# Kernel tuning notes

Hardware: AMD Instinct MI355X
Metric: run time of the kernel (lower is better)

Reference implementation:

```python
import jax, jax.numpy as jnp
import numpy as np
import math

N = 100000   # nodes
E = 1600000  # edges (avg degree 16)
D = 128      # in_dim == out_dim
H = 8        # heads
DK = D // H  # 16


def setup_inputs() -> dict:
    key = jax.random.key(0)
    ks = jax.random.split(key, 16)
    s = 1.0 / math.sqrt(D)
    inp = {
        "h": jax.random.normal(ks[0], (N, D), dtype=jnp.float32),
        "src": jax.random.randint(ks[1], (E,), 0, N, dtype=jnp.int32),
        "dst": jax.random.randint(ks[2], (E,), 0, N, dtype=jnp.int32),
        # linear params (torch Linear: y = x @ W.T + b)
        "Wk": jax.random.normal(ks[3], (D, D), dtype=jnp.float32) * s,
        "bk": jnp.zeros((D,), dtype=jnp.float32),
        "Wq": jax.random.normal(ks[4], (D, D), dtype=jnp.float32) * s,
        "bq": jnp.zeros((D,), dtype=jnp.float32),
        "Wv": jax.random.normal(ks[5], (D, D), dtype=jnp.float32) * s,
        "bv": jnp.zeros((D,), dtype=jnp.float32),
        "Wa": jax.random.normal(ks[6], (D, D), dtype=jnp.float32) * s,
        "ba": jnp.zeros((D,), dtype=jnp.float32),
        # relation params
        "rel_att": jax.random.normal(ks[7], (H, DK, DK), dtype=jnp.float32) * (1.0 / math.sqrt(DK)),
        "rel_msg": jax.random.normal(ks[8], (H, DK, DK), dtype=jnp.float32) * (1.0 / math.sqrt(DK)),
        "rel_pri": jnp.ones((H,), dtype=jnp.float32),
        "skip": jnp.ones((1,), dtype=jnp.float32),
    }
    return inp


def reference(h, src, dst, Wk, bk, Wq, bq, Wv, bv, Wa, ba, rel_att, rel_msg, rel_pri, skip):
    sqrt_dk = math.sqrt(DK)
    # per-node projections -> [N, H, DK]
    k = (h @ Wk.T + bk).reshape(N, H, DK)
    q = (h @ Wq.T + bq).reshape(N, H, DK)
    v = (h @ Wv.T + bv).reshape(N, H, DK)
    # per-relation transforms on k and v
    k = jnp.einsum('nhd,hde->nhe', k, rel_att)
    v = jnp.einsum('nhd,hde->nhe', v, rel_msg)
    # edge scores: dot(q[dst], k[src]) per head -> [E, H]
    score = jnp.einsum('ehd,ehd->eh', q[dst], k[src])
    score = score * rel_pri / sqrt_dk
    # edge softmax normalized over incoming edges of each dst node
    smax = jax.ops.segment_max(score, dst, num_segments=N)        # [N, H]
    ex = jnp.exp(score - smax[dst])                               # [E, H]
    denom = jax.ops.segment_sum(ex, dst, num_segments=N)         # [N, H]
    attn = ex / denom[dst]                                       # [E, H]
    # weighted scatter-aggregation of source values
    msg = v[src] * attn[:, :, None]                               # [E, H, DK]
    t = jax.ops.segment_sum(msg, dst, num_segments=N)             # [N, H, DK]
    t = t.reshape(N, D)
    # target-specific aggregation with learned skip gate (dropout=0 eval, norm=Identity)
    trans_out = t @ Wa.T + ba
    alpha = jax.nn.sigmoid(skip[0])
    new_h = trans_out * alpha + h * (1.0 - alpha)
    return new_h
```

## Files before the change

### kernel.cpp

```cpp
#include <hip/hip_runtime.h>
#include <hip/hip_bf16.h>
#include <math.h>

#define NN 100000
#define EE 1600000
#define DD 128
#define HH 8
#define LDW 136
#define BSH 9
#define NB 196
#define EPB 8192

typedef short short8 __attribute__((ext_vector_type(8)));
typedef float f32x4 __attribute__((ext_vector_type(4)));

__device__ __forceinline__ unsigned short f2bf(float f) {
    unsigned int u = __float_as_uint(f);
    u += 0x7fffu + ((u >> 16) & 1u);
    return (unsigned short)(u >> 16);
}
__device__ __forceinline__ float bf2f(unsigned short h) {
    return __uint_as_float((unsigned int)h << 16);
}
__device__ __forceinline__ void cvt8(const float4& a, const float4& b,
                                     short8& h8, short8& l8) {
    float vals[8] = {a.x, a.y, a.z, a.w, b.x, b.y, b.z, b.w};
    #pragma unroll
    for (int j = 0; j < 8; j++) {
        unsigned short hi = f2bf(vals[j]);
        h8[j] = (short)hi;
        l8[j] = (short)f2bf(vals[j] - bf2f(hi));
    }
}

__global__ void prep_weights(const float* __restrict__ Wq, const float* __restrict__ Wk,
                             const float* __restrict__ Wv, const float* __restrict__ Wa,
                             const float* __restrict__ bq, const float* __restrict__ bk,
                             const float* __restrict__ bv, const float* __restrict__ ba,
                             const float* __restrict__ rel_att, const float* __restrict__ rel_msg,
                             unsigned short* __restrict__ WH, unsigned short* __restrict__ WL,
                             float* __restrict__ BE) {
    int o = blockIdx.x * 256 + threadIdx.x;
    int j = o >> 7, c = o & 127;
    int which = blockIdx.y;
    float val;
    if (which == 0) {
        val = Wq[o];
        if (o < 128) BE[o] = bq[o];
    } else if (which == 3) {
        val = Wa[o];
        if (o < 128) BE[384 + o] = ba[o];
    } else {
        const float* rel = (which == 1) ? rel_att : rel_msg;
        const float* W   = (which == 1) ? Wk : Wv;
        const float* b   = (which == 1) ? bk : bv;
        int hh = j >> 4, e = j & 15;
        val = 0.f;
        #pragma unroll
        for (int d = 0; d < 16; d++)
            val += rel[hh * 256 + d * 16 + e] * W[(hh * 16 + d) * 128 + c];
        if (c == 0) {
            float bacc = 0.f;
            #pragma unroll
            for (int d = 0; d < 16; d++)
                bacc += b[hh * 16 + d] * rel[hh * 256 + d * 16 + e];
            BE[which * 128 + j] = bacc;
        }
    }
    unsigned short hi = f2bf(val);
    unsigned short lo = f2bf(val - bf2f(hi));
    WH[which * 16384 + o] = hi;
    WL[which * 16384 + o] = lo;
}

__launch_bounds__(256, 2)
__global__ void gemm_reg(const float* __restrict__ x,
                         const unsigned short* __restrict__ WH,
                         const unsigned short* __restrict__ WL,
                         const float* __restrict__ BE, int nw,
                         float* __restrict__ out0, unsigned short* __restrict__ kvout,
                         const float* __restrict__ resid, const float* __restrict__ skip) {
    __shared__ unsigned short wh[128 * LDW];
    __shared__ unsigned short wl[128 * LDW];
    int tid = threadIdx.x;
    int wv = tid >> 6, lane = tid & 63;
    int lrow = lane & 15, quad = lane >> 4;
    int base = blockIdx.x * 128;

    short8 ah[2][4], al[2][4];
    float4 fz = {0.f, 0.f, 0.f, 0.f};
    #pragma unroll
    for (int mt = 0; mt < 2; mt++) {
        int row = base + wv * 32 + mt * 16 + lrow;
        const float* xr = x + (size_t)row * 128;
        bool ok = (row < NN);
        #pragma unroll
        for (int kc = 0; kc < 4; kc++) {
            int off = kc * 32 + quad * 8;
            float4 a = ok ? *(const float4*)&xr[off] : fz;
            float4 b = ok ? *(const float4*)&xr[off + 4] : fz;
            cvt8(a, b, ah[mt][kc], al[mt][kc]);
        }
    }

    float alpha = 1.f, beta = 0.f;
    if (resid) {
        float sv = skip[0];
        alpha = 1.f / (1.f + expf(-sv));
        beta = 1.f - alpha;
    }

    for (int wi = 0; wi < nw; wi++) {
        __syncthreads();
        const unsigned short* WHp = WH + wi * 16384;
        const unsigned short* WLp = WL + wi * 16384;
        for (int i = tid; i < 128 * 16; i += 256) {
            int n = i >> 4, kq = (i & 15) << 3;
            *(uint4*)&wh[n * LDW + kq] = *(const uint4*)&WHp[n * 128 + kq];
            *(uint4*)&wl[n * LDW + kq] = *(const uint4*)&WLp[n * 128 + kq];
        }
        __syncthreads();

        f32x4 zero4 = {0.f, 0.f, 0.f, 0.f};
        f32x4 acc[2][8];
        #pragma unroll
        for (int a = 0; a < 2; a++)
            #pragma unroll
            for (int b = 0; b < 8; b++) acc[a][b] = zero4;

        #pragma unroll
        for (int kc = 0; kc < 4; kc++) {
            #pragma unroll
            for (int nt = 0; nt < 8; nt++) {
                int koff = kc * 32 + quad * 8;
                int brow = (nt * 16 + lrow) * LDW + koff;
                short8 bh = *(const short8*)&wh[brow];
                short8 bl = *(const short8*)&wl[brow];
                acc[0][nt] = __builtin_amdgcn_mfma_f32_16x16x32_bf16(ah[0][kc], bh, acc[0][nt], 0, 0, 0);
                acc[1][nt] = __builtin_amdgcn_mfma_f32_16x16x32_bf16(ah[1][kc], bh, acc[1][nt], 0, 0, 0);
                acc[0][nt] = __builtin_amdgcn_mfma_f32_16x16x32_bf16(al[0][kc], bh, acc[0][nt], 0, 0, 0);
                acc[1][nt] = __builtin_amdgcn_mfma_f32_16x16x32_bf16(al[1][kc], bh, acc[1][nt], 0, 0, 0);
                acc[0][nt] = __builtin_amdgcn_mfma_f32_16x16x32_bf16(ah[0][kc], bl, acc[0][nt], 0, 0, 0);
                acc[1][nt] = __builtin_amdgcn_mfma_f32_16x16x32_bf16(ah[1][kc], bl, acc[1][nt], 0, 0, 0);
            }
        }

        const float* be = BE + wi * 128;
        #pragma unroll
        for (int nt = 0; nt < 8; nt++) {
            int col = nt * 16 + lrow;
            float bb = be[col];
            #pragma unroll
            for (int mt = 0; mt < 2; mt++) {
                int r0 = base + wv * 32 + mt * 16 + quad * 4;
                #pragma unroll
                for (int rg = 0; rg < 4; rg++) {
                    int row = r0 + rg;
                    if (row < NN) {
                        float val = acc[mt][nt][rg] + bb;
                        if (wi == 0) {
                            if (resid) val = alpha * val + beta * resid[(size_t)row * 128 + col];
                            out0[(size_t)row * 128 + col] = val;
                        } else {
                            int pos = ((col >> 2) << 3) + ((wi - 1) << 2) + (col & 3);
                            kvout[(size_t)row * 256 + pos] = f2bf(val);
                        }
                    }
                }
            }
        }
    }
}

__global__ void bucket_hist(const int* __restrict__ dst, int* __restrict__ bcnt) {
    __shared__ int lh[NB];
    int t = threadIdx.x;
    for (int i = t; i < NB; i += 256) lh[i] = 0;
    __syncthreads();
    int base = blockIdx.x * EPB;
    int cnt = min(EPB, EE - base);
    for (int i = t; i < cnt; i += 256)
        atomicAdd(&lh[dst[base + i] >> BSH], 1);
    __syncthreads();
    for (int i = t; i < NB; i += 256)
        if (lh[i]) atomicAdd(&bcnt[i], lh[i]);
}

__global__ void bucket_scan(const int* __restrict__ bcnt, int* __restrict__ btail,
                            int* __restrict__ sbase) {
    __shared__ int buf[2][256];
    int t = threadIdx.x;
    int v = (t < NB) ? bcnt[t] : 0;
    buf[0][t] = v;
    __syncthreads();
    int sb = 0;
    #pragma unroll
    for (int d = 1; d < 256; d <<= 1) {
        int x = buf[sb][t];
        if (t >= d) x += buf[sb][t - d];
        buf[sb ^ 1][t] = x;
        __syncthreads();
        sb ^= 1;
    }
    if (t < NB) {
        int excl = buf[sb][t] - v;
        btail[t] = excl;
        sbase[t] = excl;
    }
    if (t == 0) sbase[NB] = EE;
}

__launch_bounds__(256, 1)
__global__ void bucket_scatter(const int* __restrict__ src, const int* __restrict__ dst,
                               int* __restrict__ btail, int* __restrict__ packed) {
    __shared__ int2 staged[EPB];
    __shared__ int hist[NB], lstart[NB], cursor[NB], gbase[NB];
    __shared__ int sbuf[2][256];
    int t = threadIdx.x;
    for (int i = t; i < NB; i += 256) hist[i] = 0;
    __syncthreads();
    int base = blockIdx.x * EPB;
    int cnt = min(EPB, EE - base);
    for (int i = t; i < cnt; i += 256)
        atomicAdd(&hist[dst[base + i] >> BSH], 1);
    __syncthreads();
    int v = (t < NB) ? hist[t] : 0;
    sbuf[0][t] = v;
    __syncthreads();
    int sb = 0;
    #pragma unroll
    for (int d = 1; d < 256; d <<= 1) {
        int x = sbuf[sb][t];
        if (t >= d) x += sbuf[sb][t - d];
        sbuf[sb ^ 1][t] = x;
        __syncthreads();
        sb ^= 1;
    }
    if (t < NB) {
        lstart[t] = sbuf[sb][t] - v;
        cursor[t] = sbuf[sb][t] - v;
    }
    __syncthreads();
    for (int i = t; i < cnt; i += 256) {
        int d = dst[base + i], s = src[base + i];
        int r = atomicAdd(&cursor[d >> BSH], 1);
        staged[r] = make_int2(s, d);
    }
    __syncthreads();
    for (int i = t; i < NB; i += 256) {
        int c = hist[i];
        if (c) gbase[i] = atomicAdd(&btail[i], c);
    }
    __syncthreads();
    for (int i = t; i < cnt; i += 256) {
        int2 e = staged[i];
        int b = e.y >> BSH;
        packed[gbase[b] + (i - lstart[b])] = ((e.y & 511) << 17) | e.x;
    }
}

__launch_bounds__(512, 2)
__global__ void node_sort(const int* __restrict__ packed, const int* __restrict__ sbase,
                          int* __restrict__ offs, int* __restrict__ sorted_src) {
    __shared__ int hist[512], cursor[512];
    __shared__ int scn[2][512];
    int t = threadIdx.x;
    int b = blockIdx.x;
    int s0 = sbase[b], s1 = sbase[b + 1];
    hist[t] = 0;
    __syncthreads();
    for (int e = s0 + t; e < s1; e += 512)
        atomicAdd(&hist[packed[e] >> 17], 1);
    __syncthreads();
    int v = hist[t];
    scn[0][t] = v;
    __syncthreads();
    int sb = 0;
    #pragma unroll
    for (int d = 1; d < 512; d <<= 1) {
        int x = scn[sb][t];
        if (t >= d) x += scn[sb][t - d];
        scn[sb ^ 1][t] = x;
        __syncthreads();
        sb ^= 1;
    }
    int incl = scn[sb][t];
    int node = (b << BSH) + t;
    if (node < NN) offs[node] = s0 + incl;
    cursor[t] = s0 + incl - v;
    __syncthreads();
    for (int e = s0 + t; e < s1; e += 512) {
        int p = packed[e];
        int pos = atomicAdd(&cursor[p >> 17], 1);
        sorted_src[pos] = p & 0x1FFFF;
    }
}

__launch_bounds__(256, 8)
__global__ void fused_attn(const float* __restrict__ q,
                           const unsigned short* __restrict__ kv,
                           const int* __restrict__ offs, const int* __restrict__ sorted_src,
                           const float* __restrict__ rel_pri, float* __restrict__ t) {
    int wave = threadIdx.x >> 6, lane = threadIdx.x & 63;
    int n = blockIdx.x * 4 + wave;
    if (n >= NN) return;
    int half = lane >> 5;
    int sl = lane & 31;
    int hh = sl >> 2;
    int start = (n > 0) ? offs[n - 1] : 0;
    int cnt = offs[n] - start;

    float4 q4 = *(const float4*)&q[(size_t)n * 128 + sl * 4];
    float scale = rel_pri[hh] * 0.25f * 1.44269504088896340736f;
    q4.x *= scale; q4.y *= scale; q4.z *= scale; q4.w *= scale;

    const unsigned short* kvp = kv + sl * 8;

    float4 o4 = {0.f, 0.f, 0.f, 0.f};
    float denom = 0.f;

    int nIter = (cnt + 1) >> 1;
    #pragma unroll 4
    for (int it = 0; it < nIter; it++) {
        int j = 2 * it + half;
        float wgt = (j < cnt) ? 1.f : 0.f;
        int jj = (j < cnt) ? j : (cnt - 1);
        int s = sorted_src[start + jj];
        uint4 kvb = *(const uint4*)(kvp + (size_t)s * 256);
        float p = q4.x * bf2f((unsigned short)(kvb.x & 0xffff))
                + q4.y * bf2f((unsigned short)(kvb.x >> 16))
                + q4.z * bf2f((unsigned short)(kvb.y & 0xffff))
                + q4.w * bf2f((unsigned short)(kvb.y >> 16));
        p += __shfl_xor(p, 1);
        p += __shfl_xor(p, 2);
        float e = __builtin_amdgcn_exp2f(p) * wgt;
        denom += e;
        o4.x = fmaf(bf2f((unsigned short)(kvb.z & 0xffff)), e, o4.x);
        o4.y = fmaf(bf2f((unsigned short)(kvb.z >> 16)),    e, o4.y);
        o4.z = fmaf(bf2f((unsigned short)(kvb.w & 0xffff)), e, o4.z);
        o4.w = fmaf(bf2f((unsigned short)(kvb.w >> 16)),    e, o4.w);
    }

    denom += __shfl_xor(denom, 32);
    o4.x += __shfl_xor(o4.x, 32);
    o4.y += __shfl_xor(o4.y, 32);
    o4.z += __shfl_xor(o4.z, 32);
    o4.w += __shfl_xor(o4.w, 32);

    if (half == 0) {
        float inv = (cnt > 0) ? 1.f / denom : 0.f;
        o4.x *= inv; o4.y *= inv; o4.z *= inv; o4.w *= inv;
        *(float4*)&t[(size_t)n * 128 + sl * 4] = o4;
    }
}

extern "C" void kernel_launch(void* const* d_in, const int* in_sizes, int n_in,
                              void* d_out, int out_size, void* d_ws, size_t ws_size,
                              hipStream_t stream) {
    const float* h    = (const float*)d_in[0];
    const int*   src  = (const int*)d_in[1];
    const int*   dst  = (const int*)d_in[2];
    const float* Wk   = (const float*)d_in[3];
    const float* bk   = (const float*)d_in[4];
    const float* Wq   = (const float*)d_in[5];
    const float* bq   = (const float*)d_in[6];
    const float* Wv   = (const float*)d_in[7];
    const float* bv   = (const float*)d_in[8];
    const float* Wa   = (const float*)d_in[9];
    const float* ba   = (const float*)d_in[10];
    const float* rel_att = (const float*)d_in[11];
    const float* rel_msg = (const float*)d_in[12];
    const float* rel_pri = (const float*)d_in[13];
    const float* skip    = (const float*)d_in[14];
    float* out = (float*)d_out;

    unsigned short* kvbuf = (unsigned short*)d_ws;
    float* BE   = (float*)(kvbuf + (size_t)NN * 256);
    int* scratch = (int*)(BE + 512);
    int* bcnt  = scratch;
    int* btail = bcnt + NB;
    int* sbase = btail + NB;
    int* offs  = scratch + NN;
    int* bsum  = offs + NN;
    int* sorted_src = bsum + 128;
    unsigned short* WH = (unsigned short*)(sorted_src + EE);
    unsigned short* WL = WH + 4 * 16384;
    int* packed = (int*)kvbuf;
    float* q = out;
    float* t = out;

    const int A_BLOCKS = (EE + EPB - 1) / EPB;
    const int GEMM_BLOCKS = (NN + 127) / 128;

    prep_weights<<<dim3(64, 4), 256, 0, stream>>>(Wq, Wk, Wv, Wa, bq, bk, bv, ba,
                                                  rel_att, rel_msg, WH, WL, BE);
    hipMemsetAsync(bcnt, 0, NB * sizeof(int), stream);
    bucket_hist<<<A_BLOCKS, 256, 0, stream>>>(dst, bcnt);
    bucket_scan<<<1, 256, 0, stream>>>(bcnt, btail, sbase);
    bucket_scatter<<<A_BLOCKS, 256, 0, stream>>>(src, dst, btail, packed);
    node_sort<<<NB, 512, 0, stream>>>(packed, sbase, offs, sorted_src);

    gemm_reg<<<GEMM_BLOCKS, 256, 0, stream>>>(h, WH, WL, BE, 3, q, kvbuf,
                                              nullptr, nullptr);
    fused_attn<<<(NN + 3) / 4, 256, 0, stream>>>(q, kvbuf, offs, sorted_src,
                                                 rel_pri, t);
    gemm_reg<<<GEMM_BLOCKS, 256, 0, stream>>>(t, WH + 3 * 16384, WL + 3 * 16384,
                                              BE + 384, 1, out, nullptr,
                                              h, skip);
}
```

Before: 494.8 us.

## Merge weight prep with histogram and bucket scatter with QKV GEMM launches

Weight preparation and the dst histogram now run as one launch, using block-index ranges to pick the work. When the workspace is large enough, the packed edge buffer gets its own region, so the bucket scatter and the QKV projection GEMM can share one launch and run concurrently. The attention kernel now has each wave process four nodes in sequence, which cuts the block count. These changes reduce launch overhead and idle tails, but the merged kernel's shared-memory footprint and occupancy are set by the larger of the two roles, and the dependent path only runs if the workspace is big enough.

Result: no change. 493.3 us (-0.3%).

```diff
diff --git a/kernel.cpp b/kernel.cpp
--- a/kernel.cpp
+++ b/kernel.cpp
@@ -10,6 +10,8 @@
 #define BSH 9
 #define NB 196
 #define EPB 8192
+#define A_BLOCKS 196
+#define GEMM_BLOCKS 782
 
 typedef short short8 __attribute__((ext_vector_type(8)));
 typedef float f32x4 __attribute__((ext_vector_type(4)));
@@ -33,16 +35,16 @@
     }
 }
 
-__global__ void prep_weights(const float* __restrict__ Wq, const float* __restrict__ Wk,
+__device__ __forceinline__ void prep_work(int which, int bx,
+                             const float* __restrict__ Wq, const float* __restrict__ Wk,
                              const float* __restrict__ Wv, const float* __restrict__ Wa,
                              const float* __restrict__ bq, const float* __restrict__ bk,
                              const float* __restrict__ bv, const float* __restrict__ ba,
                              const float* __restrict__ rel_att, const float* __restrict__ rel_msg,
                              unsigned short* __restrict__ WH, unsigned short* __restrict__ WL,
                              float* __restrict__ BE) {
-    int o = blockIdx.x * 256 + threadIdx.x;
+    int o = bx * 256 + threadIdx.x;
     int j = o >> 7, c = o & 127;
-    int which = blockIdx.y;
     float val;
     if (which == 0) {
         val = Wq[o];
@@ -73,19 +75,45 @@
     WL[which * 16384 + o] = lo;
 }
 
-__launch_bounds__(256, 2)
-__global__ void gemm_reg(const float* __restrict__ x,
+__global__ void prep_hist(const float* __restrict__ Wq, const float* __restrict__ Wk,
+                          const float* __restrict__ Wv, const float* __restrict__ Wa,
+                          const float* __restrict__ bq, const float* __restrict__ bk,
+                          const float* __restrict__ bv, const float* __restrict__ ba,
+                          const float* __restrict__ rel_att, const float* __restrict__ rel_msg,
+                          unsigned short* __restrict__ WH, unsigned short* __restrict__ WL,
+                          float* __restrict__ BE,
+                          const int* __restrict__ dst, int* __restrict__ bcnt) {
+    __shared__ int lh[NB];
+    int bid = blockIdx.x;
+    if (bid < 256) {
+        prep_work(bid >> 6, bid & 63, Wq, Wk, Wv, Wa, bq, bk, bv, ba,
+                  rel_att, rel_msg, WH, WL, BE);
+    } else {
+        int t = threadIdx.x;
+        for (int i = t; i < NB; i += 256) lh[i] = 0;
+        __syncthreads();
+        int base = (bid - 256) * EPB;
+        int cnt = min(EPB, EE - base);
+        for (int i = t; i < cnt; i += 256)
+            atomicAdd(&lh[dst[base + i] >> BSH], 1);
+        __syncthreads();
+        for (int i = t; i < NB; i += 256)
+            if (lh[i]) atomicAdd(&bcnt[i], lh[i]);
+    }
+}
+
+__device__ __forceinline__ void gemm_body(char* smemc, int base,
+                         const float* __restrict__ x,
                          const unsigned short* __restrict__ WH,
                          const unsigned short* __restrict__ WL,
                          const float* __restrict__ BE, int nw,
                          float* __restrict__ out0, unsigned short* __restrict__ kvout,
                          const float* __restrict__ resid, const float* __restrict__ skip) {
-    __shared__ unsigned short wh[128 * LDW];
-    __shared__ unsigned short wl[128 * LDW];
+    unsigned short* wh = (unsigned short*)smemc;
+    unsigned short* wl = wh + 128 * LDW;
     int tid = threadIdx.x;
     int wv = tid >> 6, lane = tid & 63;
     int lrow = lane & 15, quad = lane >> 4;
-    int base = blockIdx.x * 128;
 
     short8 ah[2][4], al[2][4];
     float4 fz = {0.f, 0.f, 0.f, 0.f};
@@ -172,18 +200,15 @@
     }
 }
 
-__global__ void bucket_hist(const int* __restrict__ dst, int* __restrict__ bcnt) {
-    __shared__ int lh[NB];
-    int t = threadIdx.x;
-    for (int i = t; i < NB; i += 256) lh[i] = 0;
-    __syncthreads();
-    int base = blockIdx.x * EPB;
-    int cnt = min(EPB, EE - base);
-    for (int i = t; i < cnt; i += 256)
-        atomicAdd(&lh[dst[base + i] >> BSH], 1);
-    __syncthreads();
-    for (int i = t; i < NB; i += 256)
-        if (lh[i]) atomicAdd(&bcnt[i], lh[i]);
+__launch_bounds__(256, 2)
+__global__ void gemm_reg(const float* __restrict__ x,
+                         const unsigned short* __restrict__ WH,
+                         const unsigned short* __restrict__ WL,
+                         const float* __restrict__ BE, int nw,
+                         float* __restrict__ out0, unsigned short* __restrict__ kvout,
+                         const float* __restrict__ resid, const float* __restrict__ skip) {
+    __shared__ __align__(16) char smem[69632];
+    gemm_body(smem, blockIdx.x * 128, x, WH, WL, BE, nw, out0, kvout, resid, skip);
 }
 
 __global__ void bucket_scan(const int* __restrict__ bcnt, int* __restrict__ btail,
@@ -210,35 +235,38 @@
     if (t == 0) sbase[NB] = EE;
 }
 
-__launch_bounds__(256, 1)
-__global__ void bucket_scatter(const int* __restrict__ src, const int* __restrict__ dst,
+__device__ __forceinline__ void scatter_work(char* smemc, int bid,
+                               const int* __restrict__ src, const int* __restrict__ dst,
                                int* __restrict__ btail, int* __restrict__ packed) {
-    __shared__ int2 staged[EPB];
-    __shared__ int hist[NB], lstart[NB], cursor[NB], gbase[NB];
-    __shared__ int sbuf[2][256];
+    int2* staged = (int2*)smemc;
+    int* hist   = (int*)(smemc + 65536);
+    int* lstart = hist + NB;
+    int* cursor = lstart + NB;
+    int* gbase  = cursor + NB;
+    int* sbuf   = gbase + NB;
     int t = threadIdx.x;
     for (int i = t; i < NB; i += 256) hist[i] = 0;
     __syncthreads();
-    int base = blockIdx.x * EPB;
+    int base = bid * EPB;
     int cnt = min(EPB, EE - base);
     for (int i = t; i < cnt; i += 256)
         atomicAdd(&hist[dst[base + i] >> BSH], 1);
     __syncthreads();
     int v = (t < NB) ? hist[t] : 0;
-    sbuf[0][t] = v;
+    sbuf[t] = v;
     __syncthreads();
     int sb = 0;
     #pragma unroll
     for (int d = 1; d < 256; d <<= 1) {
-        int x = sbuf[sb][t];
-        if (t >= d) x += sbuf[sb][t - d];
-        sbuf[sb ^ 1][t] = x;
+        int x = sbuf[sb * 256 + t];
+        if (t >= d) x += sbuf[sb * 256 + t - d];
+        sbuf[(sb ^ 1) * 256 + t] = x;
         __syncthreads();
         sb ^= 1;
     }
     if (t < NB) {
-        lstart[t] = sbuf[sb][t] - v;
-        cursor[t] = sbuf[sb][t] - v;
+        lstart[t] = sbuf[sb * 256 + t] - v;
+        cursor[t] = sbuf[sb * 256 + t] - v;
     }
     __syncthreads();
     for (int i = t; i < cnt; i += 256) {
@@ -257,6 +285,29 @@
         int b = e.y >> BSH;
         packed[gbase[b] + (i - lstart[b])] = ((e.y & 511) << 17) | e.x;
     }
+}
+
+__launch_bounds__(256, 1)
+__global__ void bucket_scatter(const int* __restrict__ src, const int* __restrict__ dst,
+                               int* __restrict__ btail, int* __restrict__ packed) {
+    __shared__ __align__(16) char smem[70720];
+    scatter_work(smem, blockIdx.x, src, dst, btail, packed);
+}
+
+__launch_bounds__(256, 2)
+__global__ void gemm0_scatter(const float* __restrict__ x,
+                              const unsigned short* __restrict__ WH,
+                              const unsigned short* __restrict__ WL,
+                              const float* __restrict__ BE,
+                              float* __restrict__ q, unsigned short* __restrict__ kvout,
+                              const int* __restrict__ src, const int* __restrict__ dst,
+                              int* __restrict__ btail, int* __restrict__ packed) {
+    __shared__ __align__(16) char smem[70720];
+    if (blockIdx.x < A_BLOCKS)
+        scatter_work(smem, blockIdx.x, src, dst, btail, packed);
+    else
+        gemm_body(smem, (blockIdx.x - A_BLOCKS) * 128, x, WH, WL, BE, 3,
+                  q, kvout, nullptr, nullptr);
 }
 
 __launch_bounds__(512, 2)
@@ -302,55 +353,59 @@
                            const int* __restrict__ offs, const int* __restrict__ sorted_src,
                            const float* __restrict__ rel_pri, float* __restrict__ t) {
     int wave = threadIdx.x >> 6, lane = threadIdx.x & 63;
-    int n = blockIdx.x * 4 + wave;
-    if (n >= NN) return;
     int half = lane >> 5;
     int sl = lane & 31;
     int hh = sl >> 2;
-    int start = (n > 0) ? offs[n - 1] : 0;
-    int cnt = offs[n] - start;
-
-    float4 q4 = *(const float4*)&q[(size_t)n * 128 + sl * 4];
     float scale = rel_pri[hh] * 0.25f * 1.44269504088896340736f;
-    q4.x *= scale; q4.y *= scale; q4.z *= scale; q4.w *= scale;
-
     const unsigned short* kvp = kv + sl * 8;
 
-    float4 o4 = {0.f, 0.f, 0.f, 0.f};
-    float denom = 0.f;
-
-    int nIter = (cnt + 1) >> 1;
-    #pragma unroll 4
-    for (int it = 0; it < nIter; it++) {
-        int j = 2 * it + half;
-        float wgt = (j < cnt) ? 1.f : 0.f;
-        int jj = (j < cnt) ? j : (cnt - 1);
-        int s = sorted_src[start + jj];
-        uint4 kvb = *(const uint4*)(kvp + (size_t)s * 256);
-        float p = q4.x * bf2f((unsigned short)(kvb.x & 0xffff))
-                + q4.y * bf2f((unsigned short)(kvb.x >> 16))
-                + q4.z * bf2f((unsigned short)(kvb.y & 0xffff))
-                + q4.w * bf2f((unsigned short)(kvb.y >> 16));
-        p += __shfl_xor(p, 1);
-        p += __shfl_xor(p, 2);
-        float e = __builtin_amdgcn_exp2f(p) * wgt;
-        denom += e;
-        o4.x = fmaf(bf2f((unsigned short)(kvb.z & 0xffff)), e, o4.x);
-        o4.y = fmaf(bf2f((unsigned short)(kvb.z >> 16)),    e, o4.y);
-        o4.z = fmaf(bf2f((unsigned short)(kvb.w & 0xffff)), e, o4.z);
-        o4.w = fmaf(bf2f((unsigned short)(kvb.w >> 16)),    e, o4.w);
-    }
-
-    denom += __shfl_xor(denom, 32);
-    o4.x += __shfl_xor(o4.x, 32);
-    o4.y += __shfl_xor(o4.y, 32);
-    o4.z += __shfl_xor(o4.z, 32);
-    o4.w += __shfl_xor(o4.w, 32);
-
-    if (half == 0) {
-        float inv = (cnt > 0) ? 1.f / denom : 0.f;
-        o4.x *= inv; o4.y *= inv; o4.z *= inv; o4.w *= inv;
-        *(float4*)&t[(size_t)n * 128 + sl * 4] = o4;
+    int n0 = (blockIdx.x * 4 + wave) * 4;
+    #pragma unroll 1
+    for (int ni = 0; ni < 4; ni++) {
+        int n = n0 + ni;
+        if (n >= NN) return;
+        int start = (n > 0) ? offs[n - 1] : 0;
+        int cnt = offs[n] - start;
+
+        float4 q4 = *(const float4*)&q[(size_t)n * 128 + sl * 4];
+        q4.x *= scale; q4.y *= scale; q4.z *= scale; q4.w *= scale;
+
+        float4 o4 = {0.f, 0.f, 0.f, 0.f};
+        float denom = 0.f;
+
+        int nIter = (cnt + 1) >> 1;
+        #pragma unroll 4
+        for (int it = 0; it < nIter; it++) {
+            int j = 2 * it + half;
+            float wgt = (j < cnt) ? 1.f : 0.f;
+            int jj = (j < cnt) ? j : (cnt - 1);
+            int s = sorted_src[start + jj];
+            uint4 kvb = *(const uint4*)(kvp + (size_t)s * 256);
+            float p = q4.x * bf2f((unsigned short)(kvb.x & 0xffff))
+                    + q4.y * bf2f((unsigned short)(kvb.x >> 16))
+                    + q4.z * bf2f((unsigned short)(kvb.y & 0xffff))
+                    + q4.w * bf2f((unsigned short)(kvb.y >> 16));
+            p += __shfl_xor(p, 1);
+            p += __shfl_xor(p, 2);
+            float e = __builtin_amdgcn_exp2f(p) * wgt;
+            denom += e;
+            o4.x = fmaf(bf2f((unsigned short)(kvb.z & 0xffff)), e, o4.x);
+            o4.y = fmaf(bf2f((unsigned short)(kvb.z >> 16)),    e, o4.y);
+            o4.z = fmaf(bf2f((unsigned short)(kvb.w & 0xffff)), e, o4.z);
+            o4.w = fmaf(bf2f((unsigned short)(kvb.w >> 16)),    e, o4.w);
+        }
+
+        denom += __shfl_xor(denom, 32);
+        o4.x += __shfl_xor(o4.x, 32);
+        o4.y += __shfl_xor(o4.y, 32);
+        o4.z += __shfl_xor(o4.z, 32);
+        o4.w += __shfl_xor(o4.w, 32);
+
+        if (half == 0) {
+            float inv = (cnt > 0) ? 1.f / denom : 0.f;
+            o4.x *= inv; o4.y *= inv; o4.z *= inv; o4.w *= inv;
+            *(float4*)&t[(size_t)n * 128 + sl * 4] = o4;
+        }
     }
 }
 
@@ -385,25 +440,32 @@
     int* sorted_src = bsum + 128;
     unsigned short* WH = (unsigned short*)(sorted_src + EE);
     unsigned short* WL = WH + 4 * 16384;
-    int* packed = (int*)kvbuf;
+    char* ws_end = (char*)(WL + 4 * 16384);
+    size_t used = (size_t)(ws_end - (char*)d_ws);
+    bool sep = (ws_size >= used + (size_t)EE * sizeof(int));
+    int* packed = sep ? (int*)ws_end : (int*)kvbuf;
     float* q = out;
     float* t = out;
 
-    const int A_BLOCKS = (EE + EPB - 1) / EPB;
-    const int GEMM_BLOCKS = (NN + 127) / 128;
-
-    prep_weights<<<dim3(64, 4), 256, 0, stream>>>(Wq, Wk, Wv, Wa, bq, bk, bv, ba,
-                                                  rel_att, rel_msg, WH, WL, BE);
     hipMemsetAsync(bcnt, 0, NB * sizeof(int), stream);
-    bucket_hist<<<A_BLOCKS, 256, 0, stream>>>(dst, bcnt);
+    prep_hist<<<256 + A_BLOCKS, 256, 0, stream>>>(Wq, Wk, Wv, Wa, bq, bk, bv, ba,
+                                                  rel_att, rel_msg, WH, WL, BE,
+                                                  dst, bcnt);
     bucket_scan<<<1, 256, 0, stream>>>(bcnt, btail, sbase);
-    bucket_scatter<<<A_BLOCKS, 256, 0, stream>>>(src, dst, btail, packed);
-    node_sort<<<NB, 512, 0, stream>>>(packed, sbase, offs, sorted_src);
-
-    gemm_reg<<<GEMM_BLOCKS, 256, 0, stream>>>(h, WH, WL, BE, 3, q, kvbuf,
-                                              nullptr, nullptr);
-    fused_attn<<<(NN + 3) / 4, 256, 0, stream>>>(q, kvbuf, offs, sorted_src,
-                                                 rel_pri, t);
+
+    if (sep) {
+        gemm0_scatter<<<A_BLOCKS + GEMM_BLOCKS, 256, 0, stream>>>(
+            h, WH, WL, BE, q, kvbuf, src, dst, btail, packed);
+        node_sort<<<NB, 512, 0, stream>>>(packed, sbase, offs, sorted_src);
+    } else {
+        bucket_scatter<<<A_BLOCKS, 256, 0, stream>>>(src, dst, btail, packed);
+        node_sort<<<NB, 512, 0, stream>>>(packed, sbase, offs, sorted_src);
+        gemm_reg<<<GEMM_BLOCKS, 256, 0, stream>>>(h, WH, WL, BE, 3, q, kvbuf,
+                                                  nullptr, nullptr);
+    }
+
+    fused_attn<<<(NN + 15) / 16, 256, 0, stream>>>(q, kvbuf, offs, sorted_src,
+                                                   rel_pri, t);
     gemm_reg<<<GEMM_BLOCKS, 256, 0, stream>>>(t, WH + 3 * 16384, WL + 3 * 16384,
                                               BE + 384, 1, out, nullptr,
                                               h, skip);
```
